# Optimization experiments

Hardware: AMD Instinct MI355X
Metric: run time of the kernel (lower is better)

The kernel has to match this reference:

```python
import jax, jax.numpy as jnp
import numpy as np

N, E, D, H, L, G, OUT = 16384, 65536, 64, 128, 3, 512, 128
EPS = 1e-5


def setup_inputs() -> dict:
    key = jax.random.key(0)
    ks = jax.random.split(key, 12)
    s = 0.05  # small init to keep res+ stack stable
    return {
        "x": jax.random.normal(ks[0], (N, D), jnp.float32),
        "edge_index": jax.random.randint(ks[1], (2, E), 0, N, jnp.int32),
        "edge_attr": jax.random.normal(ks[2], (E, D), jnp.float32),
        "batch": jnp.sort(jax.random.randint(ks[3], (N,), 0, G, jnp.int32)),
        # per-layer params, stacked on leading layer dim L
        "ln_scale": jnp.ones((L, D), jnp.float32),
        "ln_bias": jnp.zeros((L, D), jnp.float32),
        "W1": jax.random.normal(ks[4], (L, D, H), jnp.float32) * s,
        "b1": jnp.zeros((L, H), jnp.float32),
        "W2": jax.random.normal(ks[5], (L, H, D * D), jnp.float32) * s,
        "b2": jnp.zeros((L, D * D), jnp.float32),
        "root": jax.random.normal(ks[6], (L, D, D), jnp.float32) * s,
        "conv_b": jnp.zeros((L, D), jnp.float32),
        # head params
        "dense_W": jax.random.normal(ks[7], (D, D), jnp.float32) * s,
        "dense_b": jnp.zeros((D,), jnp.float32),
        "out_W": jax.random.normal(ks[8], (D, OUT), jnp.float32) * s,
        "out_b": jnp.zeros((OUT,), jnp.float32),
    }


def _layer_norm(h, scale, bias):
    mu = jnp.mean(h, axis=-1, keepdims=True)
    var = jnp.mean((h - mu) ** 2, axis=-1, keepdims=True)
    return (h - mu) * jax.lax.rsqrt(var + EPS) * scale + bias


def _gnn_layer(x, edge_index, edge_attr, ln_scale, ln_bias, W1, b1, W2, b2, root, conv_b):
    # DeepGCNLayer block='res+': h = conv(dropout(act(norm(x)))); return x + h
    # (dropout is identity in eval/reference)
    h = jax.nn.leaky_relu(_layer_norm(x, ln_scale, ln_bias))
    src, dst = edge_index[0], edge_index[1]
    # NNConv: per-edge DxD weight from edge MLP (MapE2NxN with LeakyReLU)
    w = jax.nn.leaky_relu(edge_attr @ W1 + b1) @ W2 + b2       # [E, D*D]
    w = w.reshape(-1, D, D)                                     # [E, D, D]
    msg = jnp.einsum('ed,edf->ef', h[src], w)                   # [E, D]
    num = jax.ops.segment_sum(msg, dst, num_segments=N)         # [N, D]
    deg = jax.ops.segment_sum(jnp.ones((msg.shape[0],), msg.dtype), dst, num_segments=N)
    agg = num / jnp.maximum(deg, 1.0)[:, None]                  # mean aggregation
    conv = agg + h @ root + conv_b                              # root weight + bias
    return x + conv


def reference(x, edge_index, edge_attr, batch, ln_scale, ln_bias, W1, b1, W2, b2,
              root, conv_b, dense_W, dense_b, out_W, out_b):
    for l in range(L):
        x = _gnn_layer(x, edge_index, edge_attr, ln_scale[l], ln_bias[l],
                       W1[l], b1[l], W2[l], b2[l], root[l], conv_b[l])
    x = x @ dense_W + dense_b
    # global_mean_pool over graphs
    num = jax.ops.segment_sum(x, batch, num_segments=G)
    cnt = jax.ops.segment_sum(jnp.ones((x.shape[0],), x.dtype), batch, num_segments=G)
    pooled = num / jnp.maximum(cnt, 1.0)[:, None]
    pooled = jax.nn.leaky_relu(pooled)
    return pooled @ out_W + out_b
```

## Files before the change

### kernel.cpp

```cpp
#include <hip/hip_runtime.h>
#include <hip/hip_bf16.h>

#define NN 16384
#define EE 65536
#define DD 64
#define HH 128
#define LL 3
#define GG 512
#define OUTD 128
#define NEG 0.01f

#define CHUNK 8192
#define KSEG 8


typedef __attribute__((ext_vector_type(8))) short short8;
typedef __attribute__((ext_vector_type(4))) float f32x4;

__device__ __forceinline__ float leaky(float x){ return x > 0.f ? x : NEG * x; }
__device__ __forceinline__ unsigned short f2bf(float f){
  union { float f; unsigned int u; } v; v.f = f;
  unsigned int r = v.u + 0x7fffu + ((v.u >> 16) & 1u);
  return (unsigned short)(r >> 16);
}

__global__ void k_deg(const int* ei, int* deg){
  int e = blockIdx.x*256 + threadIdx.x;
  if (e < EE) atomicAdd(&deg[ei[EE + e]], 1);
}
__global__ void k_cnt(const int* batch, int* cnt){
  int n = blockIdx.x*256 + threadIdx.x;
  if (n < NN) atomicAdd(&cnt[batch[n]], 1);
}
__global__ void k_scan(const int* deg, int* row_ptr){
  __shared__ int part[256];
  int t = threadIdx.x;
  int base = t*64; int s = 0;
  for (int i=0;i<64;++i) s += deg[base+i];
  part[t] = s; __syncthreads();
  for (int off=1; off<256; off<<=1){
    int v = (t>=off)?part[t-off]:0; __syncthreads();
    part[t] += v; __syncthreads();
  }
  int run = (t==0)?0:part[t-1];
  if (t==0) row_ptr[0] = 0;
  for (int i=0;i<64;++i){ run += deg[base+i]; row_ptr[base+i+1] = run; }
}
__global__ void k_fill(const int* ei, const int* row_ptr, int* cursor,
                       int* edge_id, int* src_sorted){
  int e = blockIdx.x*256 + threadIdx.x;
  if (e < EE){
    int d = ei[EE + e];
    int pos = row_ptr[d] + atomicAdd(&cursor[d], 1);
    edge_id[pos] = e;
    src_sorted[pos] = ei[e];
  }
}

__global__ void k_prep_ea(const float* ea, unsigned short* eab){
  int i = blockIdx.x*256 + threadIdx.x;
  eab[i] = f2bf(ea[i]);
}
__global__ void k_prep_w1t(const float* W1, unsigned short* W1T){
  int i = blockIdx.x*256 + threadIdx.x;
  int l = i >> 13, r = i & 8191;
  int j = r >> 6, d = r & 63;
  W1T[i] = f2bf(W1[(size_t)l*DD*HH + d*HH + j]);
}

__global__ void k_ln(const float* x, const float* scale, const float* bias, float* h, int l){
  int t = threadIdx.x, lane = t & 63, nl = t >> 6;
  int n = blockIdx.x*4 + nl;
  float v = x[(size_t)n*DD + lane];
  float s = v;
  for (int m=1;m<64;m<<=1) s += __shfl_xor(s, m, 64);
  float mu = s * (1.0f/64.0f);
  float dv = v - mu;
  float q = dv*dv;
  for (int m=1;m<64;m<<=1) q += __shfl_xor(q, m, 64);
  float var = q * (1.0f/64.0f);
  float w = dv * rsqrtf(var + 1e-5f) * scale[l*DD + lane] + bias[l*DD + lane];
  h[(size_t)n*DD + lane] = leaky(w);
}

__global__ __launch_bounds__(256, 2)
void k_edge_mlp(const unsigned short* eab, const unsigned short* W1T, const float* b1,
                unsigned short* ug, int l){
  __shared__ __align__(16) unsigned short a_lds[128][72];
  __shared__ __align__(16) unsigned short b_lds[128][72];
  __shared__ __align__(16) unsigned short c_lds[128][136];
  int t = threadIdx.x;
  int e0 = blockIdx.x * 128;
  {
    int row = t >> 1, col = (t & 1) * 32;
    const float4* sa = (const float4*)(eab + (size_t)(e0 + row)*DD + col);
    const float4* sb = (const float4*)(W1T + (size_t)l*HH*DD + (size_t)row*DD + col);
    #pragma unroll
    for (int i=0;i<4;++i){
      *(float4*)&a_lds[row][col + 8*i] = sa[i];
      *(float4*)&b_lds[row][col + 8*i] = sb[i];
    }
  }
  __syncthreads();
  int wave = t >> 6, lane = t & 63;
  int m0 = (wave >> 1) * 64, j0 = (wave & 1) * 64;
  int lr = lane & 15, lq = lane >> 4;
  f32x4 acc[4][4];
  #pragma unroll
  for (int a=0;a<4;++a)
    #pragma unroll
    for (int b=0;b<4;++b) acc[a][b] = (f32x4){0.f,0.f,0.f,0.f};
  #pragma unroll
  for (int ks=0; ks<2; ++ks){
    short8 av[4];
    #pragma unroll
    for (int mt=0; mt<4; ++mt) av[mt] = *(const short8*)&a_lds[m0 + mt*16 + lr][ks*32 + lq*8];
    #pragma unroll
    for (int jt=0; jt<4; ++jt){
      short8 bv = *(const short8*)&b_lds[j0 + jt*16 + lr][ks*32 + lq*8];
      #pragma unroll
      for (int mt=0; mt<4; ++mt)
        acc[mt][jt] = __builtin_amdgcn_mfma_f32_16x16x32_bf16(av[mt], bv, acc[mt][jt], 0, 0, 0);
    }
  }
  #pragma unroll
  for (int mt=0; mt<4; ++mt)
    #pragma unroll
    for (int jt=0; jt<4; ++jt){
      int col = j0 + jt*16 + lr;
      float bj = b1[l*HH + col];
      #pragma unroll
      for (int r=0; r<4; ++r){
        int row = m0 + mt*16 + lq*4 + r;
        c_lds[row][col] = f2bf(leaky(acc[mt][jt][r] + bj));
      }
    }
  __syncthreads();
  {
    int row = t >> 1, half = t & 1;
    float4* dst = (float4*)(ug + (size_t)(e0 + row)*HH + half*64);
    #pragma unroll
    for (int i=0;i<8;++i) dst[i] = *(const float4*)&c_lds[row][half*64 + 8*i];
  }
}

__global__ void k_w2t(const float* W2, unsigned short* W2T, int l){
  int idx = blockIdx.x*256 + threadIdx.x;
  int f = idx >> 13, c = idx & 8191;
  int kd = 128*((c>>3)&63) + 64*(c>>12) + 8*((c>>9)&7) + (c&7);
  W2T[idx] = f2bf(W2[(size_t)l*HH*DD*DD + (size_t)kd*DD + f]);
}

__global__ __launch_bounds__(256, 2)
void k_sbuild2(const unsigned short* ug, const float* h, const int* row_ptr,
               const int* edge_id, const int* src_sorted,
               unsigned short* S, float* Hs, int chunk_base){
  int t = threadIdx.x, wave = t >> 6, lane = t & 63;
  int nloc = blockIdx.x*4 + wave;
  int n = chunk_base + nloc;
  int r0 = row_ptr[n], r1 = row_ptr[n+1];
  float acc0[64], acc1[64];
  #pragma unroll
  for (int d=0; d<64; ++d){ acc0[d] = 0.f; acc1[d] = 0.f; }
  float hs = 0.f;
  int pos = r0;
  for (; pos + 2 <= r1; pos += 2){
    int e0 = edge_id[pos],    e1 = edge_id[pos+1];
    int s0 = src_sorted[pos], s1 = src_sorted[pos+1];
    float hv0 = h[(size_t)s0*DD + lane];
    float hv1 = h[(size_t)s1*DD + lane];
    unsigned int q0 = *(const unsigned int*)(ug + (size_t)e0*HH + 2*lane);
    unsigned int q1 = *(const unsigned int*)(ug + (size_t)e1*HH + 2*lane);
    float u00 = __uint_as_float(q0 << 16), u01 = __uint_as_float(q0 & 0xFFFF0000u);
    float u10 = __uint_as_float(q1 << 16), u11 = __uint_as_float(q1 & 0xFFFF0000u);
    hs += hv0 + hv1;
    int h0 = __float_as_int(hv0), h1 = __float_as_int(hv1);
    #pragma unroll
    for (int d=0; d<64; ++d){
      float sh0 = __int_as_float(__builtin_amdgcn_readlane(h0, d));
      float sh1 = __int_as_float(__builtin_amdgcn_readlane(h1, d));
      acc0[d] += u00*sh0; acc0[d] += u10*sh1;
      acc1[d] += u01*sh0; acc1[d] += u11*sh1;
    }
  }
  if (pos < r1){
    int e = edge_id[pos];
    int s = src_sorted[pos];
    float hv = h[(size_t)s*DD + lane];
    unsigned int up = *(const unsigned int*)(ug + (size_t)e*HH + 2*lane);
    float u0 = __uint_as_float(up << 16);
    float u1 = __uint_as_float(up & 0xFFFF0000u);
    hs += hv;
    int hvi = __float_as_int(hv);
    #pragma unroll
    for (int d=0; d<64; ++d){
      float sh = __int_as_float(__builtin_amdgcn_readlane(hvi, d));
      acc0[d] += u0 * sh;
      acc1[d] += u1 * sh;
    }
  }
  float4* Srow = (float4*)(S + (size_t)nloc*8192);
  #pragma unroll
  for (int k2=0; k2<2; ++k2){
    union { unsigned int u[32]; float4 v[8]; } buf;
    #pragma unroll
    for (int i=0;i<32;++i){
      float a0 = k2 ? acc1[2*i]   : acc0[2*i];
      float a1 = k2 ? acc1[2*i+1] : acc0[2*i+1];
      buf.u[i] = (unsigned int)f2bf(a0) | ((unsigned int)f2bf(a1) << 16);
    }
    #pragma unroll
    for (int i=0;i<8;++i)
      Srow[(k2*8 + i)*64 + lane] = buf.v[i];
  }
  Hs[(size_t)n*DD + lane] = hs;
}

__global__ __launch_bounds__(256, 4)
void k_gemm(const unsigned short* S, const unsigned short* W2T,
            float* num_part, int chunk_base){
  __shared__ __align__(16) unsigned short a_lds[64][72];
  __shared__ __align__(16) unsigned short b_lds[64][72];
  int t = threadIdx.x;
  int wave = t >> 6, lane = t & 63;
  int rowblk = blockIdx.x, kseg = blockIdx.y;
  int lr = lane & 15, lq = lane >> 4;
  f32x4 acc[4];
  #pragma unroll
  for (int b=0;b<4;++b) acc[b] = (f32x4){0.f,0.f,0.f,0.f};
  int m0 = wave * 16;
  for (int it = 0; it < 16; ++it){
    int kbase = kseg*1024 + it*64;
    #pragma unroll
    for (int ii=0; ii<2; ++ii){
      int idx = t + 256*ii;
      int r = idx >> 3, c8 = (idx & 7) << 3;
      float4 v = *(const float4*)(S + (size_t)(rowblk*64 + r)*8192 + kbase + c8);
      *(float4*)&a_lds[r][c8] = v;
    }
    #pragma unroll
    for (int ii=0; ii<2; ++ii){
      int idx = t + 256*ii;
      int r = idx >> 3, c8 = (idx & 7) << 3;
      float4 v = *(const float4*)(W2T + (size_t)r*8192 + kbase + c8);
      *(float4*)&b_lds[r][c8] = v;
    }
    __syncthreads();
    #pragma unroll
    for (int kk=0; kk<64; kk+=32){
      short8 av = *(const short8*)&a_lds[m0 + lr][kk + lq*8];
      #pragma unroll
      for (int ft=0; ft<4; ++ft){
        short8 bv = *(const short8*)&b_lds[ft*16 + lr][kk + lq*8];
        acc[ft] = __builtin_amdgcn_mfma_f32_16x16x32_bf16(av, bv, acc[ft], 0, 0, 0);
      }
    }
    __syncthreads();
  }
  float* dstp = num_part + (size_t)kseg*NN*DD;
  #pragma unroll
  for (int ft=0; ft<4; ++ft)
    #pragma unroll
    for (int r=0; r<4; ++r){
      int m = m0 + lq*4 + r;
      int f = ft*16 + lr;
      int n = chunk_base + rowblk*64 + m;
      dstp[(size_t)n*DD + f] = acc[ft][r];
    }
}

__global__ void k_update(float* x, const float* num_part, const float* h, const float* Hs,
                         const int* deg, const float* root, const float* b2,
                         const float* conv_b, int l){
  __shared__ float rl[64][64];
  __shared__ float b2l[64][64];
  __shared__ float hrow[4][64];
  __shared__ float hsrow[4][64];
  int t = threadIdx.x;
  int f = t & 63, nl = t >> 6;
  for (int idx=t; idx<4096; idx+=256){
    rl[idx>>6][idx&63]  = root[(size_t)l*4096 + idx];
    b2l[idx>>6][idx&63] = b2[(size_t)l*4096 + idx];
  }
  int n = blockIdx.x*4 + nl;
  hrow[nl][f]  = h[(size_t)n*DD + f];
  hsrow[nl][f] = Hs[(size_t)n*DD + f];
  __syncthreads();
  float dg = (float)deg[n]; if (dg < 1.f) dg = 1.f;
  float nsum = 0.f;
  #pragma unroll
  for (int p=0; p<KSEG; ++p) nsum += num_part[(size_t)p*NN*DD + (size_t)n*DD + f];
  float acc = x[(size_t)n*DD + f] + nsum/dg + conv_b[l*DD + f];
  #pragma unroll
  for (int d=0; d<64; ++d)
    acc += hrow[nl][d]*rl[d][f] + hsrow[nl][d]*b2l[d][f];
  x[(size_t)n*DD + f] = acc;
}

__global__ void k_dense_pool(const float* x, const float* dW, const float* db,
                             const int* batch, float* pooled){
  __shared__ float wl[64][64];
  __shared__ float xrow[4][64];
  int t = threadIdx.x;
  int f = t & 63, nl = t >> 6;
  for (int idx=t; idx<4096; idx+=256) wl[idx>>6][idx&63] = dW[idx];
  int n = blockIdx.x*4 + nl;
  xrow[nl][f] = x[(size_t)n*DD + f];
  __syncthreads();
  float acc = db[f];
  #pragma unroll
  for (int d=0; d<64; ++d) acc += xrow[nl][d]*wl[d][f];
  atomicAdd(&pooled[(size_t)batch[n]*DD + f], acc);
}

__global__ void k_final(const float* pooled, const int* cnt, const float* oW,
                        const float* ob, float* out){
  __shared__ float p[64];
  int g = blockIdx.x, t = threadIdx.x;
  if (t < 64){
    float c = (float)cnt[g]; if (c < 1.f) c = 1.f;
    p[t] = leaky(pooled[(size_t)g*DD + t] / c);
  }
  __syncthreads();
  float acc = ob[t];
  #pragma unroll
  for (int f=0; f<64; ++f) acc += p[f]*oW[(size_t)f*OUTD + t];
  out[(size_t)g*OUTD + t] = acc;
}

__global__ void k_diag(float* out, float val, int n){
  int i = blockIdx.x*256 + threadIdx.x;
  if (i < n) out[i] = (i==0) ? val : 0.f;
}

extern "C" void kernel_launch(void* const* d_in, const int* in_sizes, int n_in,
                              void* d_out, int out_size, void* d_ws, size_t ws_size,
                              hipStream_t stream){
  const float* x_in  = (const float*)d_in[0];
  const int*   ei    = (const int*)d_in[1];
  const float* ea    = (const float*)d_in[2];
  const int*   batch = (const int*)d_in[3];
  const float* ln_s  = (const float*)d_in[4];
  const float* ln_b  = (const float*)d_in[5];
  const float* W1    = (const float*)d_in[6];
  const float* b1    = (const float*)d_in[7];
  const float* W2    = (const float*)d_in[8];
  const float* b2    = (const float*)d_in[9];
  const float* root  = (const float*)d_in[10];
  const float* convb = (const float*)d_in[11];
  const float* dW    = (const float*)d_in[12];
  const float* db    = (const float*)d_in[13];
  const float* oW    = (const float*)d_in[14];
  const float* ob    = (const float*)d_in[15];
  float* out = (float*)d_out;

  char* ws = (char*)d_ws;
  size_t off = 0;
  auto alloc = [&](size_t bytes)->char*{
    char* p = ws + off; off = (off + bytes + 255) & ~(size_t)255; return p;
  };
  float* x_cur  = (float*)alloc((size_t)NN*DD*4);
  float* h      = (float*)alloc((size_t)NN*DD*4);
  unsigned short* ug  = (unsigned short*)alloc((size_t)EE*HH*2);
  float* num_part = (float*)alloc((size_t)KSEG*NN*DD*4);
  float* Hs     = (float*)alloc((size_t)NN*DD*4);
  unsigned short* S   = (unsigned short*)alloc((size_t)CHUNK*8192*2);
  unsigned short* W2T = (unsigned short*)alloc((size_t)8192*64*2);
  unsigned short* eab = (unsigned short*)alloc((size_t)EE*DD*2);
  unsigned short* W1T = (unsigned short*)alloc((size_t)LL*HH*DD*2);
  int* deg     = (int*)alloc((size_t)NN*4);
  int* row_ptr = (int*)alloc((size_t)(NN+1)*4);
  int* cursor  = (int*)alloc((size_t)NN*4);
  int* edge_id = (int*)alloc((size_t)EE*4);
  int* src_sorted = (int*)alloc((size_t)EE*4);
  int* cnt     = (int*)alloc((size_t)GG*4);
  float* pooled= (float*)alloc((size_t)GG*DD*4);
  size_t needed = off;
  if (ws_size < needed){
    k_diag<<<(out_size+255)/256, 256, 0, stream>>>(out, (float)ws_size, out_size);
    return;
  }

  hipMemsetAsync(deg, 0, (size_t)NN*4, stream);
  hipMemsetAsync(cursor, 0, (size_t)NN*4, stream);
  hipMemsetAsync(cnt, 0, (size_t)GG*4, stream);
  hipMemsetAsync(pooled, 0, (size_t)GG*DD*4, stream);
  hipMemcpyAsync(x_cur, x_in, (size_t)NN*DD*4, hipMemcpyDeviceToDevice, stream);

  k_deg <<<EE/256, 256, 0, stream>>>(ei, deg);
  k_cnt <<<NN/256, 256, 0, stream>>>(batch, cnt);
  k_scan<<<1, 256, 0, stream>>>(deg, row_ptr);
  k_fill<<<EE/256, 256, 0, stream>>>(ei, row_ptr, cursor, edge_id, src_sorted);
  k_prep_ea <<<(EE*DD)/256, 256, 0, stream>>>(ea, eab);
  k_prep_w1t<<<(LL*HH*DD)/256, 256, 0, stream>>>(W1, W1T);

  for (int l=0; l<LL; ++l){
    k_ln      <<<NN/4, 256, 0, stream>>>(x_cur, ln_s, ln_b, h, l);
    k_edge_mlp<<<EE/128, 256, 0, stream>>>(eab, W1T, b1, ug, l);
    k_w2t     <<<(8192*64)/256, 256, 0, stream>>>(W2, W2T, l);
    for (int c=0; c<NN/CHUNK; ++c){
      k_sbuild2<<<CHUNK/4, 256, 0, stream>>>(ug, h, row_ptr, edge_id, src_sorted, S, Hs, c*CHUNK);
      k_gemm   <<<dim3(CHUNK/64, KSEG), 256, 0, stream>>>(S, W2T, num_part, c*CHUNK);
    }
    k_update<<<NN/4, 256, 0, stream>>>(x_cur, num_part, h, Hs, deg, root, b2, convb, l);
  }
  k_dense_pool<<<NN/4, 256, 0, stream>>>(x_cur, dW, db, batch, pooled);
  k_final     <<<GG, 128, 0, stream>>>(pooled, cnt, oW, ob, out);
}
```

Measured before the change: 638.6 us.

## Merge setup and per-layer kernels, unroll sbuild by four, widen GEMM K tile

Several small setup kernels and the memset/memcpy calls are merged into one init kernel, one degree/count kernel and one conversion kernel. The conversion kernel now transposes and converts W2 for all layers up front instead of once per layer. LayerNorm and the edge MLP are launched as a single grid, the message-building loop processes four edges per iteration instead of two, and the GEMM loads 128-wide K tiles so it synchronises half as often. The aim is fewer launches and more memory-level parallelism, in exchange for higher register pressure in sbuild and more LDS use in the GEMM.

```diff
diff --git a/kernel.cpp b/kernel.cpp
--- a/kernel.cpp
+++ b/kernel.cpp
@@ -24,13 +24,19 @@
   return (unsigned short)(r >> 16);
 }
 
-__global__ void k_deg(const int* ei, int* deg){
+__global__ void k_init(const float* x_in, float* x_cur, int* deg, int* cursor,
+                       int* cnt, float* pooled){
+  int i = blockIdx.x*256 + threadIdx.x;
+  x_cur[i] = x_in[i];
+  if (i < NN){ deg[i] = 0; cursor[i] = 0; }
+  if (i < GG) cnt[i] = 0;
+  if (i < GG*DD) pooled[i] = 0.f;
+}
+
+__global__ void k_degcnt(const int* ei, const int* batch, int* deg, int* cnt){
   int e = blockIdx.x*256 + threadIdx.x;
-  if (e < EE) atomicAdd(&deg[ei[EE + e]], 1);
-}
-__global__ void k_cnt(const int* batch, int* cnt){
-  int n = blockIdx.x*256 + threadIdx.x;
-  if (n < NN) atomicAdd(&cnt[batch[n]], 1);
+  atomicAdd(&deg[ei[EE + e]], 1);
+  if (e < NN) atomicAdd(&cnt[batch[e]], 1);
 }
 __global__ void k_scan(const int* deg, int* row_ptr){
   __shared__ int part[256];
@@ -57,40 +63,52 @@
   }
 }
 
-__global__ void k_prep_ea(const float* ea, unsigned short* eab){
-  int i = blockIdx.x*256 + threadIdx.x;
-  eab[i] = f2bf(ea[i]);
-}
-__global__ void k_prep_w1t(const float* W1, unsigned short* W1T){
-  int i = blockIdx.x*256 + threadIdx.x;
-  int l = i >> 13, r = i & 8191;
-  int j = r >> 6, d = r & 63;
-  W1T[i] = f2bf(W1[(size_t)l*DD*HH + d*HH + j]);
-}
-
-__global__ void k_ln(const float* x, const float* scale, const float* bias, float* h, int l){
-  int t = threadIdx.x, lane = t & 63, nl = t >> 6;
-  int n = blockIdx.x*4 + nl;
-  float v = x[(size_t)n*DD + lane];
-  float s = v;
-  for (int m=1;m<64;m<<=1) s += __shfl_xor(s, m, 64);
-  float mu = s * (1.0f/64.0f);
-  float dv = v - mu;
-  float q = dv*dv;
-  for (int m=1;m<64;m<<=1) q += __shfl_xor(q, m, 64);
-  float var = q * (1.0f/64.0f);
-  float w = dv * rsqrtf(var + 1e-5f) * scale[l*DD + lane] + bias[l*DD + lane];
-  h[(size_t)n*DD + lane] = leaky(w);
+#define CV_A (EE*DD)
+#define CV_B (LL*HH*DD)
+#define CV_C (LL*64*8192)
+__global__ void k_convert(const float* ea, const float* W1, const float* W2,
+                          unsigned short* eab, unsigned short* W1T, unsigned short* W2T){
+  int idx = blockIdx.x*256 + threadIdx.x;
+  if (idx < CV_A){
+    eab[idx] = f2bf(ea[idx]);
+  } else if (idx < CV_A + CV_B){
+    int i = idx - CV_A;
+    int l = i >> 13, r = i & 8191;
+    int j = r >> 6, d = r & 63;
+    W1T[i] = f2bf(W1[(size_t)l*DD*HH + d*HH + j]);
+  } else {
+    int i = idx - CV_A - CV_B;
+    int l = i >> 19, rem = i & ((1<<19)-1);
+    int f = rem >> 13, c = rem & 8191;
+    int kd = 128*((c>>3)&63) + 64*(c>>12) + 8*((c>>9)&7) + (c&7);
+    W2T[i] = f2bf(W2[(size_t)l*HH*DD*DD + (size_t)kd*DD + f]);
+  }
 }
 
 __global__ __launch_bounds__(256, 2)
-void k_edge_mlp(const unsigned short* eab, const unsigned short* W1T, const float* b1,
-                unsigned short* ug, int l){
+void k_lnmlp(const float* x, const float* scale, const float* bias, float* h,
+             const unsigned short* eab, const unsigned short* W1T, const float* b1,
+             unsigned short* ug, int l){
   __shared__ __align__(16) unsigned short a_lds[128][72];
   __shared__ __align__(16) unsigned short b_lds[128][72];
   __shared__ __align__(16) unsigned short c_lds[128][136];
   int t = threadIdx.x;
-  int e0 = blockIdx.x * 128;
+  if (blockIdx.x < NN/4){
+    int lane = t & 63, nl = t >> 6;
+    int n = blockIdx.x*4 + nl;
+    float v = x[(size_t)n*DD + lane];
+    float s = v;
+    for (int m=1;m<64;m<<=1) s += __shfl_xor(s, m, 64);
+    float mu = s * (1.0f/64.0f);
+    float dv = v - mu;
+    float q = dv*dv;
+    for (int m=1;m<64;m<<=1) q += __shfl_xor(q, m, 64);
+    float var = q * (1.0f/64.0f);
+    float w = dv * rsqrtf(var + 1e-5f) * scale[l*DD + lane] + bias[l*DD + lane];
+    h[(size_t)n*DD + lane] = leaky(w);
+    return;
+  }
+  int e0 = (blockIdx.x - NN/4) * 128;
   {
     int row = t >> 1, col = (t & 1) * 32;
     const float4* sa = (const float4*)(eab + (size_t)(e0 + row)*DD + col);
@@ -142,13 +160,6 @@
     #pragma unroll
     for (int i=0;i<8;++i) dst[i] = *(const float4*)&c_lds[row][half*64 + 8*i];
   }
-}
-
-__global__ void k_w2t(const float* W2, unsigned short* W2T, int l){
-  int idx = blockIdx.x*256 + threadIdx.x;
-  int f = idx >> 13, c = idx & 8191;
-  int kd = 128*((c>>3)&63) + 64*(c>>12) + 8*((c>>9)&7) + (c&7);
-  W2T[idx] = f2bf(W2[(size_t)l*HH*DD*DD + (size_t)kd*DD + f]);
 }
 
 __global__ __launch_bounds__(256, 2)
@@ -164,26 +175,37 @@
   for (int d=0; d<64; ++d){ acc0[d] = 0.f; acc1[d] = 0.f; }
   float hs = 0.f;
   int pos = r0;
-  for (; pos + 2 <= r1; pos += 2){
-    int e0 = edge_id[pos],    e1 = edge_id[pos+1];
-    int s0 = src_sorted[pos], s1 = src_sorted[pos+1];
+  for (; pos + 4 <= r1; pos += 4){
+    int e0 = edge_id[pos],   e1 = edge_id[pos+1],   e2 = edge_id[pos+2],   e3 = edge_id[pos+3];
+    int s0 = src_sorted[pos],s1 = src_sorted[pos+1],s2 = src_sorted[pos+2],s3 = src_sorted[pos+3];
     float hv0 = h[(size_t)s0*DD + lane];
     float hv1 = h[(size_t)s1*DD + lane];
+    float hv2 = h[(size_t)s2*DD + lane];
+    float hv3 = h[(size_t)s3*DD + lane];
     unsigned int q0 = *(const unsigned int*)(ug + (size_t)e0*HH + 2*lane);
     unsigned int q1 = *(const unsigned int*)(ug + (size_t)e1*HH + 2*lane);
+    unsigned int q2 = *(const unsigned int*)(ug + (size_t)e2*HH + 2*lane);
+    unsigned int q3 = *(const unsigned int*)(ug + (size_t)e3*HH + 2*lane);
     float u00 = __uint_as_float(q0 << 16), u01 = __uint_as_float(q0 & 0xFFFF0000u);
     float u10 = __uint_as_float(q1 << 16), u11 = __uint_as_float(q1 & 0xFFFF0000u);
-    hs += hv0 + hv1;
+    float u20 = __uint_as_float(q2 << 16), u21 = __uint_as_float(q2 & 0xFFFF0000u);
+    float u30 = __uint_as_float(q3 << 16), u31 = __uint_as_float(q3 & 0xFFFF0000u);
+    hs += hv0 + hv1 + hv2 + hv3;
     int h0 = __float_as_int(hv0), h1 = __float_as_int(hv1);
+    int h2 = __float_as_int(hv2), h3 = __float_as_int(hv3);
     #pragma unroll
     for (int d=0; d<64; ++d){
       float sh0 = __int_as_float(__builtin_amdgcn_readlane(h0, d));
       float sh1 = __int_as_float(__builtin_amdgcn_readlane(h1, d));
-      acc0[d] += u00*sh0; acc0[d] += u10*sh1;
-      acc1[d] += u01*sh0; acc1[d] += u11*sh1;
-    }
-  }
-  if (pos < r1){
+      float sh2 = __int_as_float(__builtin_amdgcn_readlane(h2, d));
+      float sh3 = __int_as_float(__builtin_amdgcn_readlane(h3, d));
+      acc0[d] += u00*sh0; acc1[d] += u01*sh0;
+      acc0[d] += u10*sh1; acc1[d] += u11*sh1;
+      acc0[d] += u20*sh2; acc1[d] += u21*sh2;
+      acc0[d] += u30*sh3; acc1[d] += u31*sh3;
+    }
+  }
+  for (; pos < r1; ++pos){
     int e = edge_id[pos];
     int s = src_sorted[pos];
     float hv = h[(size_t)s*DD + lane];
@@ -219,8 +241,8 @@
 __global__ __launch_bounds__(256, 4)
 void k_gemm(const unsigned short* S, const unsigned short* W2T,
             float* num_part, int chunk_base){
-  __shared__ __align__(16) unsigned short a_lds[64][72];
-  __shared__ __align__(16) unsigned short b_lds[64][72];
+  __shared__ __align__(16) unsigned short a_lds[64][136];
+  __shared__ __align__(16) unsigned short b_lds[64][136];
   int t = threadIdx.x;
   int wave = t >> 6, lane = t & 63;
   int rowblk = blockIdx.x, kseg = blockIdx.y;
@@ -229,25 +251,20 @@
   #pragma unroll
   for (int b=0;b<4;++b) acc[b] = (f32x4){0.f,0.f,0.f,0.f};
   int m0 = wave * 16;
-  for (int it = 0; it < 16; ++it){
-    int kbase = kseg*1024 + it*64;
-    #pragma unroll
-    for (int ii=0; ii<2; ++ii){
-      int idx = t + 256*ii;
-      int r = idx >> 3, c8 = (idx & 7) << 3;
-      float4 v = *(const float4*)(S + (size_t)(rowblk*64 + r)*8192 + kbase + c8);
-      *(float4*)&a_lds[r][c8] = v;
-    }
-    #pragma unroll
-    for (int ii=0; ii<2; ++ii){
-      int idx = t + 256*ii;
-      int r = idx >> 3, c8 = (idx & 7) << 3;
-      float4 v = *(const float4*)(W2T + (size_t)r*8192 + kbase + c8);
-      *(float4*)&b_lds[r][c8] = v;
+  int r = t >> 2, q = t & 3;
+  for (int it = 0; it < 8; ++it){
+    int kbase = kseg*1024 + it*128;
+    {
+      const float4* sa = (const float4*)(S + (size_t)(rowblk*64 + r)*8192 + kbase);
+      const float4* sb = (const float4*)(W2T + (size_t)r*8192 + kbase);
+      float4* da = (float4*)&a_lds[r][0];
+      float4* db = (float4*)&b_lds[r][0];
+      #pragma unroll
+      for (int i=0;i<4;++i){ da[q + 4*i] = sa[q + 4*i]; db[q + 4*i] = sb[q + 4*i]; }
     }
     __syncthreads();
     #pragma unroll
-    for (int kk=0; kk<64; kk+=32){
+    for (int kk=0; kk<128; kk+=32){
       short8 av = *(const short8*)&a_lds[m0 + lr][kk + lq*8];
       #pragma unroll
       for (int ft=0; ft<4; ++ft){
@@ -261,11 +278,11 @@
   #pragma unroll
   for (int ft=0; ft<4; ++ft)
     #pragma unroll
-    for (int r=0; r<4; ++r){
-      int m = m0 + lq*4 + r;
+    for (int rr=0; rr<4; ++rr){
+      int m = m0 + lq*4 + rr;
       int f = ft*16 + lr;
       int n = chunk_base + rowblk*64 + m;
-      dstp[(size_t)n*DD + f] = acc[ft][r];
+      dstp[(size_t)n*DD + f] = acc[ft][rr];
     }
 }
 
@@ -365,7 +382,7 @@
   float* num_part = (float*)alloc((size_t)KSEG*NN*DD*4);
   float* Hs     = (float*)alloc((size_t)NN*DD*4);
   unsigned short* S   = (unsigned short*)alloc((size_t)CHUNK*8192*2);
-  unsigned short* W2T = (unsigned short*)alloc((size_t)8192*64*2);
+  unsigned short* W2T = (unsigned short*)alloc((size_t)LL*8192*64*2);
   unsigned short* eab = (unsigned short*)alloc((size_t)EE*DD*2);
   unsigned short* W1T = (unsigned short*)alloc((size_t)LL*HH*DD*2);
   int* deg     = (int*)alloc((size_t)NN*4);
@@ -381,26 +398,17 @@
     return;
   }
 
-  hipMemsetAsync(deg, 0, (size_t)NN*4, stream);
-  hipMemsetAsync(cursor, 0, (size_t)NN*4, stream);
-  hipMemsetAsync(cnt, 0, (size_t)GG*4, stream);
-  hipMemsetAsync(pooled, 0, (size_t)GG*DD*4, stream);
-  hipMemcpyAsync(x_cur, x_in, (size_t)NN*DD*4, hipMemcpyDeviceToDevice, stream);
-
-  k_deg <<<EE/256, 256, 0, stream>>>(ei, deg);
-  k_cnt <<<NN/256, 256, 0, stream>>>(batch, cnt);
-  k_scan<<<1, 256, 0, stream>>>(deg, row_ptr);
-  k_fill<<<EE/256, 256, 0, stream>>>(ei, row_ptr, cursor, edge_id, src_sorted);
-  k_prep_ea <<<(EE*DD)/256, 256, 0, stream>>>(ea, eab);
-  k_prep_w1t<<<(LL*HH*DD)/256, 256, 0, stream>>>(W1, W1T);
+  k_init   <<<NN*DD/256, 256, 0, stream>>>(x_in, x_cur, deg, cursor, cnt, pooled);
+  k_degcnt <<<EE/256, 256, 0, stream>>>(ei, batch, deg, cnt);
+  k_scan   <<<1, 256, 0, stream>>>(deg, row_ptr);
+  k_fill   <<<EE/256, 256, 0, stream>>>(ei, row_ptr, cursor, edge_id, src_sorted);
+  k_convert<<<(CV_A+CV_B+CV_C)/256, 256, 0, stream>>>(ea, W1, W2, eab, W1T, W2T);
 
   for (int l=0; l<LL; ++l){
-    k_ln      <<<NN/4, 256, 0, stream>>>(x_cur, ln_s, ln_b, h, l);
-    k_edge_mlp<<<EE/128, 256, 0, stream>>>(eab, W1T, b1, ug, l);
-    k_w2t     <<<(8192*64)/256, 256, 0, stream>>>(W2, W2T, l);
+    k_lnmlp<<<NN/4 + EE/128, 256, 0, stream>>>(x_cur, ln_s, ln_b, h, eab, W1T, b1, ug, l);
     for (int c=0; c<NN/CHUNK; ++c){
       k_sbuild2<<<CHUNK/4, 256, 0, stream>>>(ug, h, row_ptr, edge_id, src_sorted, S, Hs, c*CHUNK);
-      k_gemm   <<<dim3(CHUNK/64, KSEG), 256, 0, stream>>>(S, W2T, num_part, c*CHUNK);
+      k_gemm   <<<dim3(CHUNK/64, KSEG), 256, 0, stream>>>(S, W2T + (size_t)l*8192*64, num_part, c*CHUNK);
     }
     k_update<<<NN/4, 256, 0, stream>>>(x_cur, num_part, h, Hs, deg, root, b2, convb, l);
   }
```

Measured after the change: 609.4 us. -4.6%, faster.
